# Kernel optimization log

Hardware: AMD Instinct MI355X
Metric: run time of the kernel (lower is better)

Reference implementation:

```python
import jax, jax.numpy as jnp
import numpy as np

CONF = 0.25
IOU = 0.7
MAX_DET = 300
IMG_H = 1280
IMG_W = 1280
KPT_SHAPE = (17, 3)
MAX_NMS = 3000
BS = 16
N_ANCH = 33600  # (1280/8)^2 + (1280/16)^2 + (1280/32)^2


def setup_inputs() -> dict:
    key = jax.random.key(0)
    k1, k2, k3, k4 = jax.random.split(key, 4)
    # realistic YOLO head outputs: centers in image, positive w/h, conf in (0,1)
    cxy = jax.random.uniform(k1, (BS, 2, N_ANCH)) * jnp.array([IMG_W, IMG_H], jnp.float32).reshape(1, 2, 1)
    wh = jax.random.uniform(k2, (BS, 2, N_ANCH)) * 200.0 + 4.0
    conf = jax.random.uniform(k3, (BS, 1, N_ANCH))
    kpts = jax.random.uniform(k4, (BS, 51, N_ANCH)) * float(IMG_W)
    preds = jnp.concatenate([cxy, wh, conf, kpts], axis=1).astype(jnp.float32)
    return {"preds": preds}


def _pairwise_iou(boxes):
    # boxes: [M, 4] xyxy
    area = (boxes[:, 2] - boxes[:, 0]) * (boxes[:, 3] - boxes[:, 1])
    lt = jnp.maximum(boxes[:, None, :2], boxes[None, :, :2])
    rb = jnp.minimum(boxes[:, None, 2:], boxes[None, :, 2:])
    wh = jnp.clip(rb - lt, 0.0)
    inter = wh[..., 0] * wh[..., 1]
    return inter / (area[:, None] + area[None, :] - inter + 1e-9)


def _nms_keep(boxes, valid):
    # greedy NMS over score-descending boxes; returns bool keep mask [M]
    M = boxes.shape[0]
    idx = jnp.arange(M)
    supp = (_pairwise_iou(boxes) > IOU) & (idx[None, :] > idx[:, None])

    def body(i, keep):
        # row i suppresses later boxes only if it is itself kept
        return keep & ~(supp[i] & keep[i])

    return jax.lax.fori_loop(0, M, body, valid)


def _per_image(boxes_xywh, scores, kpts):
    # boxes_xywh: [N,4], scores: [N], kpts: [N,51]
    valid = scores > CONF
    masked = jnp.where(valid, scores, -1.0)
    order = jnp.argsort(-masked)[:MAX_NMS]  # top max_nms by score, desc
    b = boxes_xywh[order]
    sc = scores[order]
    kp = kpts[order]
    v = valid[order]
    # xywh -> xyxy with clip to image bounds
    cx, cy, w, h = b[:, 0], b[:, 1], b[:, 2], b[:, 3]
    x1 = jnp.clip(cx - w / 2, 0.0, IMG_W)
    y1 = jnp.clip(cy - h / 2, 0.0, IMG_H)
    x2 = jnp.clip(cx + w / 2, 0.0, IMG_W)
    y2 = jnp.clip(cy + h / 2, 0.0, IMG_H)
    bxy = jnp.stack([x1, y1, x2, y2], axis=-1)
    # faithful to original _clip_coords quirk: only channels 0 and 1 of the 51 clipped
    kp = kp.at[:, 0].set(jnp.clip(kp[:, 0], 0.0, IMG_W))
    kp = kp.at[:, 1].set(jnp.clip(kp[:, 1], 0.0, IMG_H))
    keep = _nms_keep(bxy, v)
    rank = jnp.cumsum(keep) - 1
    sel = keep & (rank < MAX_DET)
    tgt = jnp.where(sel, rank, MAX_DET)  # dropped rows scatter to slot MAX_DET (sliced off)
    ob = jnp.zeros((MAX_DET + 1, 4), bxy.dtype).at[tgt].set(jnp.where(sel[:, None], bxy, 0.0))[:MAX_DET]
    osc = jnp.zeros((MAX_DET + 1, 1), sc.dtype).at[tgt].set(jnp.where(sel[:, None], sc[:, None], 0.0))[:MAX_DET]
    okp = jnp.zeros((MAX_DET + 1, 51), kp.dtype).at[tgt].set(jnp.where(sel[:, None], kp, 0.0))[:MAX_DET]
    return ob, osc, okp


def reference(preds):
    bs = preds.shape[0]
    x = jnp.transpose(preds, (0, 2, 1))  # [bs, N, 56]
    ob, osc, okp = jax.vmap(_per_image)(x[..., :4], x[..., 4], x[..., 5:])
    return ob, osc, okp.reshape(bs, MAX_DET, *KPT_SHAPE)
```

## Files before the change

kernel.cpp:

```cpp
#include <hip/hip_runtime.h>
#include <stdint.h>

#define N_ANCH 33600
#define BS 16
#define NCH 56
#define MAX_NMS 3000
#define MAX_DET 300
#define CONF_T 0.25f
#define IOU_T 0.7f
#define IMG 1280.0f
#define NW 47
#define NBINS 4096
#define HIST_BINS 4097
#define CAP 4096
#define WCAP 4096
#define WC_STRIDE 16

#define OFF_CAND 0
#define OFF_WL   (OFF_CAND + BS*CAP*8)
#define OFF_META (OFF_WL + BS*WCAP*4)
#define OFF_BOX  ((OFF_META + BS*MAX_NMS*8 + 15) & ~15)
#define OFF_WC   (OFF_BOX + BS*MAX_NMS*16)
#define OFF_GBM  (OFF_WC + BS*WC_STRIDE*4)

__device__ __forceinline__ int score_bucket(float c, uint32_t* bits_out) {
    if (!(c > CONF_T)) { *bits_out = 0u; return 0; }
    uint32_t bits = __float_as_uint(c);
    *bits_out = bits;
    int bucket = (int)(bits >> 12) - 0x3E800 + 1;
    bucket = bucket < 1 ? 1 : (bucket > NBINS ? NBINS : bucket);
    return bucket;
}

__device__ __forceinline__ float iou_pair(float4 bi, float ai, float4 bj) {
    float aj  = (bj.z - bj.x) * (bj.w - bj.y);
    float ltx = fmaxf(bi.x, bj.x), lty = fmaxf(bi.y, bj.y);
    float rbx = fminf(bi.z, bj.z), rby = fminf(bi.w, bj.w);
    float wx  = fmaxf(rbx - ltx, 0.f), wy = fmaxf(rby - lty, 0.f);
    float inter = wx * wy;
    return inter / (ai + aj - inter + 1e-9f);
}

__device__ __forceinline__ unsigned long long readlane64(unsigned long long v, int lane) {
    uint32_t lo = (uint32_t)v, hi = (uint32_t)(v >> 32);
    uint32_t rlo = __builtin_amdgcn_readlane(lo, lane);
    uint32_t rhi = __builtin_amdgcn_readlane(hi, lane);
    return ((unsigned long long)rhi << 32) | (unsigned long long)rlo;
}

__global__ void __launch_bounds__(1024)
k_phase1(const float* __restrict__ preds,
         unsigned long long* __restrict__ cand,
         unsigned int* __restrict__ wlist, int* __restrict__ wcount,
         int2* __restrict__ gbm) {
    __shared__ int hl[HIST_BINS];
    __shared__ int st[HIST_BINS];
    __shared__ int part[256];
    __shared__ int suf[256];
    __shared__ int ldsB, ldsM, ldsWc;
    const int b = blockIdx.x, t = threadIdx.x;
    if (t == 0) ldsWc = 0;
    for (int i = t; i < HIST_BINS; i += 1024) hl[i] = 0;
    __syncthreads();
    const float4* conf4 = (const float4*)(preds + (size_t)b * NCH * N_ANCH + 4 * N_ANCH);
    for (int a4 = t; a4 < N_ANCH / 4; a4 += 1024) {
        float4 c4 = conf4[a4];
        uint32_t bits;
        int bk;
        bk = score_bucket(c4.x, &bits); if (bk > 0) atomicAdd(&hl[bk], 1);
        bk = score_bucket(c4.y, &bits); if (bk > 0) atomicAdd(&hl[bk], 1);
        bk = score_bucket(c4.z, &bits); if (bk > 0) atomicAdd(&hl[bk], 1);
        bk = score_bucket(c4.w, &bits); if (bk > 0) atomicAdd(&hl[bk], 1);
    }
    __syncthreads();
    if (t < 256) {
        int s = 0;
        for (int k = 0; k < 16; k++) s += hl[1 + t * 16 + k];
        part[t] = s;
    }
    __syncthreads();
    if (t == 0) {
        int run = 0;
        for (int i = 255; i >= 0; i--) { suf[i] = run; run += part[i]; }
        if (run < MAX_NMS) { ldsB = 1; ldsM = run; }
    }
    __syncthreads();
    if (t < 256) {
        int run = suf[t];
        bool maycross = (run < MAX_NMS) && (run + part[t] >= MAX_NMS);
        bool done = false;
        for (int k = 15; k >= 0; k--) {
            int bin = 1 + t * 16 + k;
            st[bin] = run;
            run += hl[bin];
            if (maycross && !done && run >= MAX_NMS) { ldsB = bin; ldsM = run; done = true; }
        }
    }
    __syncthreads();
    const int B = ldsB;
    if (t < 256) {
        for (int k = 0; k < 16; k++) {
            int bin = 1 + t * 16 + k;
            int c = hl[bin], s = st[bin];
            if (c > 0 && bin >= B && s < MAX_NMS) {
                int idx = atomicAdd(&ldsWc, 1);
                wlist[b * WCAP + idx] = (unsigned int)s | ((unsigned int)c << 16);
            }
        }
    }
    __syncthreads();
    for (int a4 = t; a4 < N_ANCH / 4; a4 += 1024) {
        float4 c4 = conf4[a4];
        float cv[4] = {c4.x, c4.y, c4.z, c4.w};
        #pragma unroll
        for (int q = 0; q < 4; q++) {
            uint32_t bits;
            int bucket = score_bucket(cv[q], &bits);
            if (bucket >= B && bucket > 0) {
                int pos = atomicAdd(&st[bucket], 1);
                if (pos < CAP) {
                    int a = a4 * 4 + q;
                    cand[b * CAP + pos] =
                        ((unsigned long long)bits << 32) | (uint32_t)(~(uint32_t)a);
                }
            }
        }
    }
    if (t == 0) {
        wcount[b * WC_STRIDE] = ldsWc;
        gbm[b] = make_int2(ldsB, ldsM);
    }
}

__global__ void k_rank(const float* __restrict__ preds,
                       const unsigned long long* __restrict__ cand,
                       const unsigned int* __restrict__ wlist,
                       const int* __restrict__ wcount,
                       uint2* __restrict__ meta, float4* __restrict__ box_ws) {
    const int b = blockIdx.x;
    const int wc = wcount[b * WC_STRIDE];
    const int wv = blockIdx.y * (blockDim.x >> 6) + (threadIdx.x >> 6);
    const int lane = threadIdx.x & 63;
    const int wstride = gridDim.y * (blockDim.x >> 6);
    const float* pr = preds + (size_t)b * NCH * N_ANCH;
    for (int e = wv; e < wc; e += wstride) {
        unsigned int ent = wlist[b * WCAP + e];
        int s = (int)(ent & 0xffffu);
        int n = (int)(ent >> 16);
        if (s + n > CAP) n = CAP - s;
        const unsigned long long* seg = cand + b * CAP + s;
        for (int i = lane; i < n; i += 64) {
            unsigned long long ke = seg[i];
            int r = 0;
            for (int j = 0; j < n; j++) r += (seg[j] > ke);
            int pos = s + r;
            if (pos < MAX_NMS) {
                int oi = (int)(~(uint32_t)ke);
                uint32_t sbits = (uint32_t)(ke >> 32);
                float cx = pr[0 * N_ANCH + oi], cy = pr[1 * N_ANCH + oi];
                float w  = pr[2 * N_ANCH + oi], h  = pr[3 * N_ANCH + oi];
                float4 bx;
                bx.x = fminf(fmaxf(cx - w * 0.5f, 0.f), IMG);
                bx.y = fminf(fmaxf(cy - h * 0.5f, 0.f), IMG);
                bx.z = fminf(fmaxf(cx + w * 0.5f, 0.f), IMG);
                bx.w = fminf(fmaxf(cy + h * 0.5f, 0.f), IMG);
                box_ws[b * MAX_NMS + pos] = bx;
                meta[b * MAX_NMS + pos] = make_uint2((unsigned int)oi, sbits);
            }
        }
    }
}

__global__ void __launch_bounds__(1024)
k_nmskpt(const float* __restrict__ preds, const float4* __restrict__ box_ws,
         const uint2* __restrict__ meta, const int2* __restrict__ gbm,
         float* __restrict__ out) {
    __shared__ float4 lbox[MAX_NMS];
    __shared__ float4 kbox[MAX_DET];
    __shared__ float  karea[MAX_DET];
    __shared__ int    lsel[MAX_DET];
    __shared__ int    koi[MAX_DET];
    __shared__ unsigned long long pres[NW];
    __shared__ unsigned long long diag[64];
    __shared__ unsigned long long keptmask_sh;
    const int b = blockIdx.x, t = threadIdx.x;
    const int M = gbm[b].y;
    const int Mc = M < MAX_NMS ? M : MAX_NMS;
    for (int j = t; j < Mc; j += 1024) lbox[j] = box_ws[b * MAX_NMS + j];
    for (int j = Mc + t; j < MAX_NMS; j += 1024) lbox[j] = make_float4(0.f, 0.f, 0.f, 0.f);
    if (t < NW) {
        int base = t * 64;
        int lo = Mc - base;
        unsigned long long inv = (lo <= 0) ? ~0ull : (lo >= 64 ? 0ull : ~((1ull << lo) - 1ull));
        pres[t] = inv;
    }
    __syncthreads();
    int kc = 0;
    const int nch = (Mc + 63) >> 6;
    for (int c = 0; c < nch && kc < MAX_DET; c++) {
        int base = c * 64;
        if (t < 64) diag[t] = 0ull;
        __syncthreads();
        {
            int jl = t >> 4, kk = t & 15;
            int j = base + jl;
            if (j < MAX_NMS && kc > 0) {
                float4 bj = lbox[j];
                bool sup = false;
                for (int kidx = kk; kidx < kc; kidx += 16) {
                    if (iou_pair(kbox[kidx], karea[kidx], bj) > IOU_T) { sup = true; break; }
                }
                if (sup) atomicOr(&pres[c], 1ull << jl);
            }
        }
        {
            int il = t >> 4;
            int j0 = (t & 15) * 4;
            int i = base + il;
            if (i < MAX_NMS) {
                float4 bi = lbox[i];
                float ai = (bi.z - bi.x) * (bi.w - bi.y);
                unsigned long long m = 0ull;
                for (int q = 0; q < 4; q++) {
                    int jl = j0 + q, j = base + jl;
                    if (j > i && j < MAX_NMS) {
                        if (iou_pair(bi, ai, lbox[j]) > IOU_T) m |= 1ull << jl;
                    }
                }
                if (m) atomicOr(&diag[il], m);
            }
        }
        __syncthreads();
        if (t < 64) {
            unsigned long long mydiag = diag[t];
            unsigned long long s = pres[c];
            unsigned long long keptm = 0ull;
            int room = MAX_DET - kc;
            int jmax = MAX_NMS - base; if (jmax > 64) jmax = 64;
            for (int bb = 0; bb < jmax; bb++) {
                if (!((s >> bb) & 1ull)) {
                    s |= readlane64(mydiag, bb);
                    keptm |= 1ull << bb;
                    if (--room == 0) break;
                }
            }
            if (t == 0) keptmask_sh = keptm;
        }
        __syncthreads();
        unsigned long long keptm = keptmask_sh;
        if (t < 64 && ((keptm >> t) & 1ull)) {
            int pos = kc + __popcll(keptm & ((1ull << t) - 1ull));
            float4 bx = lbox[base + t];
            kbox[pos] = bx;
            karea[pos] = (bx.z - bx.x) * (bx.w - bx.y);
            lsel[pos] = base + t;
        }
        kc += __popcll(keptm);
        __syncthreads();
    }
    float* ob  = out;
    float* osc = out + BS * MAX_DET * 4;
    for (int r = t; r < MAX_DET; r += 1024) {
        int det = b * MAX_DET + r;
        if (r < kc) {
            float4 bx = kbox[r];
            ob[det * 4 + 0] = bx.x; ob[det * 4 + 1] = bx.y;
            ob[det * 4 + 2] = bx.z; ob[det * 4 + 3] = bx.w;
            uint2 mt = meta[b * MAX_NMS + lsel[r]];
            osc[det] = __uint_as_float(mt.y);
            koi[r] = (int)mt.x;
        } else {
            ob[det * 4 + 0] = 0.f; ob[det * 4 + 1] = 0.f;
            ob[det * 4 + 2] = 0.f; ob[det * 4 + 3] = 0.f;
            osc[det] = 0.f;
        }
    }
    __syncthreads();
    float* okp = out + BS * MAX_DET * 5;
    const float* pr = preds + (size_t)b * NCH * N_ANCH;
    for (int idx = t; idx < MAX_DET * 51; idx += 1024) {
        int r = idx / 51, lane = idx - r * 51;
        float v = 0.f;
        if (r < kc) {
            int oi = koi[r];
            v = pr[(size_t)(5 + lane) * N_ANCH + oi];
            if (lane < 2) v = fminf(fmaxf(v, 0.f), IMG);
        }
        okp[(size_t)b * MAX_DET * 51 + idx] = v;
    }
}

extern "C" void kernel_launch(void* const* d_in, const int* in_sizes, int n_in,
                              void* d_out, int out_size, void* d_ws, size_t ws_size,
                              hipStream_t stream) {
    const float* preds = (const float*)d_in[0];
    float* out = (float*)d_out;
    char* ws = (char*)d_ws;
    unsigned long long* cand = (unsigned long long*)(ws + OFF_CAND);
    unsigned int* wlist = (unsigned int*)(ws + OFF_WL);
    uint2* meta = (uint2*)(ws + OFF_META);
    float4* box = (float4*)(ws + OFF_BOX);
    int* wcount = (int*)(ws + OFF_WC);
    int2* gbm = (int2*)(ws + OFF_GBM);

    k_phase1<<<BS, 1024, 0, stream>>>(preds, cand, wlist, wcount, gbm);
    k_rank<<<dim3(BS, 32), 256, 0, stream>>>(preds, cand, wlist, wcount, meta, box);
    k_nmskpt<<<BS, 1024, 0, stream>>>(preds, box, meta, gbm, out);
}
```

Before: 260.1 us.

## Split keypoint gather into wide kernel, cache conf in registers, bound NMS by M

Phase 1 now keeps its confidence float4 loads in registers (9 per thread) between the histogram pass and the scatter pass, so the confidence row is not read from global memory twice. The NMS kernel now bounds its loops by the actual candidate count instead of MAX_NMS and no longer zero-fills unused shared boxes. The keypoint gather moves out of the 16-block NMS kernel into a separate kernel spread over many blocks, with selected anchor indices passed through a workspace array. This trades an extra launch and a small global round trip for much wider parallelism on the scattered gather, plus higher register pressure in phase 1.

```diff
diff --git a/kernel.cpp b/kernel.cpp
--- a/kernel.cpp
+++ b/kernel.cpp
@@ -15,6 +15,7 @@
 #define CAP 4096
 #define WCAP 4096
 #define WC_STRIDE 16
+#define NIT 9
 
 #define OFF_CAND 0
 #define OFF_WL   (OFF_CAND + BS*CAP*8)
@@ -22,6 +23,7 @@
 #define OFF_BOX  ((OFF_META + BS*MAX_NMS*8 + 15) & ~15)
 #define OFF_WC   (OFF_BOX + BS*MAX_NMS*16)
 #define OFF_GBM  (OFF_WC + BS*WC_STRIDE*4)
+#define OFF_FOI  (OFF_GBM + BS*8)
 
 __device__ __forceinline__ int score_bucket(float c, uint32_t* bits_out) {
     if (!(c > CONF_T)) { *bits_out = 0u; return 0; }
@@ -63,14 +65,20 @@
     for (int i = t; i < HIST_BINS; i += 1024) hl[i] = 0;
     __syncthreads();
     const float4* conf4 = (const float4*)(preds + (size_t)b * NCH * N_ANCH + 4 * N_ANCH);
-    for (int a4 = t; a4 < N_ANCH / 4; a4 += 1024) {
-        float4 c4 = conf4[a4];
-        uint32_t bits;
-        int bk;
-        bk = score_bucket(c4.x, &bits); if (bk > 0) atomicAdd(&hl[bk], 1);
-        bk = score_bucket(c4.y, &bits); if (bk > 0) atomicAdd(&hl[bk], 1);
-        bk = score_bucket(c4.z, &bits); if (bk > 0) atomicAdd(&hl[bk], 1);
-        bk = score_bucket(c4.w, &bits); if (bk > 0) atomicAdd(&hl[bk], 1);
+    float4 rc[NIT];
+    #pragma unroll
+    for (int it = 0; it < NIT; it++) {
+        int a4 = t + it * 1024;
+        if (a4 < N_ANCH / 4) {
+            float4 c4 = conf4[a4];
+            rc[it] = c4;
+            uint32_t bits;
+            int bk;
+            bk = score_bucket(c4.x, &bits); if (bk > 0) atomicAdd(&hl[bk], 1);
+            bk = score_bucket(c4.y, &bits); if (bk > 0) atomicAdd(&hl[bk], 1);
+            bk = score_bucket(c4.z, &bits); if (bk > 0) atomicAdd(&hl[bk], 1);
+            bk = score_bucket(c4.w, &bits); if (bk > 0) atomicAdd(&hl[bk], 1);
+        }
     }
     __syncthreads();
     if (t < 256) {
@@ -109,19 +117,23 @@
         }
     }
     __syncthreads();
-    for (int a4 = t; a4 < N_ANCH / 4; a4 += 1024) {
-        float4 c4 = conf4[a4];
-        float cv[4] = {c4.x, c4.y, c4.z, c4.w};
-        #pragma unroll
-        for (int q = 0; q < 4; q++) {
-            uint32_t bits;
-            int bucket = score_bucket(cv[q], &bits);
-            if (bucket >= B && bucket > 0) {
-                int pos = atomicAdd(&st[bucket], 1);
-                if (pos < CAP) {
-                    int a = a4 * 4 + q;
-                    cand[b * CAP + pos] =
-                        ((unsigned long long)bits << 32) | (uint32_t)(~(uint32_t)a);
+    #pragma unroll
+    for (int it = 0; it < NIT; it++) {
+        int a4 = t + it * 1024;
+        if (a4 < N_ANCH / 4) {
+            float4 c4 = rc[it];
+            float cv[4] = {c4.x, c4.y, c4.z, c4.w};
+            #pragma unroll
+            for (int q = 0; q < 4; q++) {
+                uint32_t bits;
+                int bucket = score_bucket(cv[q], &bits);
+                if (bucket >= B && bucket > 0) {
+                    int pos = atomicAdd(&st[bucket], 1);
+                    if (pos < CAP) {
+                        int a = a4 * 4 + q;
+                        cand[b * CAP + pos] =
+                            ((unsigned long long)bits << 32) | (uint32_t)(~(uint32_t)a);
+                    }
                 }
             }
         }
@@ -172,14 +184,12 @@
 }
 
 __global__ void __launch_bounds__(1024)
-k_nmskpt(const float* __restrict__ preds, const float4* __restrict__ box_ws,
-         const uint2* __restrict__ meta, const int2* __restrict__ gbm,
-         float* __restrict__ out) {
+k_nms(const float4* __restrict__ box_ws, const uint2* __restrict__ meta,
+      const int2* __restrict__ gbm, int* __restrict__ foi, float* __restrict__ out) {
     __shared__ float4 lbox[MAX_NMS];
     __shared__ float4 kbox[MAX_DET];
     __shared__ float  karea[MAX_DET];
     __shared__ int    lsel[MAX_DET];
-    __shared__ int    koi[MAX_DET];
     __shared__ unsigned long long pres[NW];
     __shared__ unsigned long long diag[64];
     __shared__ unsigned long long keptmask_sh;
@@ -187,7 +197,6 @@
     const int M = gbm[b].y;
     const int Mc = M < MAX_NMS ? M : MAX_NMS;
     for (int j = t; j < Mc; j += 1024) lbox[j] = box_ws[b * MAX_NMS + j];
-    for (int j = Mc + t; j < MAX_NMS; j += 1024) lbox[j] = make_float4(0.f, 0.f, 0.f, 0.f);
     if (t < NW) {
         int base = t * 64;
         int lo = Mc - base;
@@ -204,7 +213,7 @@
         {
             int jl = t >> 4, kk = t & 15;
             int j = base + jl;
-            if (j < MAX_NMS && kc > 0) {
+            if (j < Mc && kc > 0) {
                 float4 bj = lbox[j];
                 bool sup = false;
                 for (int kidx = kk; kidx < kc; kidx += 16) {
@@ -217,13 +226,13 @@
             int il = t >> 4;
             int j0 = (t & 15) * 4;
             int i = base + il;
-            if (i < MAX_NMS) {
+            if (i < Mc) {
                 float4 bi = lbox[i];
                 float ai = (bi.z - bi.x) * (bi.w - bi.y);
                 unsigned long long m = 0ull;
                 for (int q = 0; q < 4; q++) {
                     int jl = j0 + q, j = base + jl;
-                    if (j > i && j < MAX_NMS) {
+                    if (j > i && j < Mc) {
                         if (iou_pair(bi, ai, lbox[j]) > IOU_T) m |= 1ull << jl;
                     }
                 }
@@ -236,7 +245,7 @@
             unsigned long long s = pres[c];
             unsigned long long keptm = 0ull;
             int room = MAX_DET - kc;
-            int jmax = MAX_NMS - base; if (jmax > 64) jmax = 64;
+            int jmax = Mc - base; if (jmax > 64) jmax = 64;
             for (int bb = 0; bb < jmax; bb++) {
                 if (!((s >> bb) & 1ull)) {
                     s |= readlane64(mydiag, bb);
@@ -268,25 +277,30 @@
             ob[det * 4 + 2] = bx.z; ob[det * 4 + 3] = bx.w;
             uint2 mt = meta[b * MAX_NMS + lsel[r]];
             osc[det] = __uint_as_float(mt.y);
-            koi[r] = (int)mt.x;
+            foi[det] = (int)mt.x;
         } else {
             ob[det * 4 + 0] = 0.f; ob[det * 4 + 1] = 0.f;
             ob[det * 4 + 2] = 0.f; ob[det * 4 + 3] = 0.f;
             osc[det] = 0.f;
-        }
-    }
-    __syncthreads();
+            foi[det] = -1;
+        }
+    }
+}
+
+__global__ void k_kpt(const float* __restrict__ preds, const int* __restrict__ foi,
+                      float* __restrict__ out) {
+    int g = blockIdx.x * blockDim.x + threadIdx.x;
+    int det = g >> 6, lane = g & 63;
+    if (det >= BS * MAX_DET || lane >= 51) return;
+    int b = det / MAX_DET;
     float* okp = out + BS * MAX_DET * 5;
-    const float* pr = preds + (size_t)b * NCH * N_ANCH;
-    for (int idx = t; idx < MAX_DET * 51; idx += 1024) {
-        int r = idx / 51, lane = idx - r * 51;
-        float v = 0.f;
-        if (r < kc) {
-            int oi = koi[r];
-            v = pr[(size_t)(5 + lane) * N_ANCH + oi];
-            if (lane < 2) v = fminf(fmaxf(v, 0.f), IMG);
-        }
-        okp[(size_t)b * MAX_DET * 51 + idx] = v;
+    int oi = foi[det];
+    if (oi >= 0) {
+        float v = preds[(size_t)b * NCH * N_ANCH + (size_t)(5 + lane) * N_ANCH + oi];
+        if (lane < 2) v = fminf(fmaxf(v, 0.f), IMG);
+        okp[det * 51 + lane] = v;
+    } else {
+        okp[det * 51 + lane] = 0.f;
     }
 }
 
@@ -302,8 +316,10 @@
     float4* box = (float4*)(ws + OFF_BOX);
     int* wcount = (int*)(ws + OFF_WC);
     int2* gbm = (int2*)(ws + OFF_GBM);
+    int* foi = (int*)(ws + OFF_FOI);
 
     k_phase1<<<BS, 1024, 0, stream>>>(preds, cand, wlist, wcount, gbm);
     k_rank<<<dim3(BS, 32), 256, 0, stream>>>(preds, cand, wlist, wcount, meta, box);
-    k_nmskpt<<<BS, 1024, 0, stream>>>(preds, box, meta, gbm, out);
-}
+    k_nms<<<BS, 1024, 0, stream>>>(box, meta, gbm, foi, out);
+    k_kpt<<<(BS * MAX_DET * 64 + 255) / 256, 256, 0, stream>>>(preds, foi, out);
+}
```

New measurement: 229.4 us. 1.13x faster.
